# Optimization experiments

Measured on AMD Instinct MI355X. Metric: run time of the kernel, lower is better.

The kernel has to match this reference:

```python
import jax, jax.numpy as jnp
import numpy as np

TWO_PI = 2.0 * np.pi
B, S_IN, S_OUT, K, HID = 1024, 4096, 4096, 8, 512
EPS = 1e-6


def setup_inputs() -> dict:
    key = jax.random.key(0)
    k1, k2, k3, k4, k5, k6, k7, k8 = jax.random.split(key, 8)
    x_in = jax.random.uniform(k1, (B, S_OUT), dtype=jnp.float32) * TWO_PI
    x_passive = jax.random.normal(k2, (B, S_IN), dtype=jnp.float32)
    log_density = jax.random.normal(k3, (B, 1), dtype=jnp.float32)
    # MLP params (nn.Linear default-ish init scale)
    lim1 = 1.0 / np.sqrt(S_IN)
    lim2 = 1.0 / np.sqrt(HID)
    w1 = jax.random.uniform(k4, (S_IN, HID), jnp.float32, -lim1, lim1)
    b1 = jax.random.uniform(k5, (HID,), jnp.float32, -lim1, lim1)
    w2 = jax.random.uniform(k6, (HID, S_OUT * 3 * K), jnp.float32, -lim2, lim2)
    b2 = jax.random.uniform(k7, (S_OUT * 3 * K,), jnp.float32, -lim2, lim2)
    phase_shift = jax.random.uniform(k8, (1,), jnp.float32)
    return {"x_in": x_in, "x_passive": x_passive, "log_density": log_density,
            "w1": w1, "b1": b1, "w2": w2, "b2": b2, "phase_shift": phase_shift}


def reference(x_in, x_passive, log_density, w1, b1, w2, b2, phase_shift):
    # normalise network input with global mean / (unbiased) std, as torch does
    xn = (x_passive - x_passive.mean()) / x_passive.std(ddof=1)
    # dense network: Linear -> tanh -> Linear -> tanh (final_activation=activation)
    net = jnp.tanh(jnp.tanh(xn @ w1 + b1) @ w2 + b2)            # (B, S*3K)
    net = net.reshape(-1, S_OUT, 3 * K)
    h_raw, w_raw, d_raw = net[..., :K], net[..., K:2 * K], net[..., 2 * K:]
    h_norm = jax.nn.softmax(h_raw, axis=2) * TWO_PI              # (B,S,K)
    w_norm = jax.nn.softmax(w_raw, axis=2) * TWO_PI
    d_norm = jax.nn.softplus(d_raw)
    bshape = (h_norm.shape[0], S_OUT, 1)
    x_kp = jnp.concatenate([jnp.full(bshape, -EPS, h_norm.dtype),
                            jnp.cumsum(w_norm, axis=2)], axis=2)  # (B,S,K+1)
    phi_kp = jnp.concatenate([jnp.zeros(bshape, h_norm.dtype),
                              jnp.cumsum(h_norm, axis=2)], axis=2)
    x = x_in[..., None]                                          # (B,S,1)
    # searchsorted (left) per element: count of knots strictly less than x, minus 1
    k_ind = jnp.sum(x_kp < x, axis=2, keepdims=True) - 1         # (B,S,1) int
    k_ind = jnp.clip(k_ind, 0, K - 1)
    g = lambda a, i: jnp.take_along_axis(a, i, axis=2)
    w_k = g(w_norm, k_ind)
    h_k = g(h_norm, k_ind)
    s_k = h_k / w_k
    d_k = g(d_norm, k_ind)
    d_kp1 = g(d_norm, (k_ind + 1) % K)
    x_km1 = g(x_kp, k_ind)
    phi_km1 = g(phi_kp, k_ind)
    alpha = (x - x_km1) / w_k
    a1m = alpha * (1.0 - alpha)
    denom = s_k + (d_kp1 + d_k - 2.0 * s_k) * a1m
    phi_out = (phi_km1 + h_k * (s_k * alpha ** 2 + d_k * a1m) / denom)[..., 0]
    phi_out = (phi_out + phase_shift) % TWO_PI                   # (B,S)
    grad = s_k ** 2 * (d_kp1 * alpha ** 2 + 2.0 * s_k * a1m
                       + d_k * (1.0 - alpha) ** 2) / denom ** 2  # (B,S,1)
    log_density = log_density - jnp.log(grad).sum(axis=1)        # (B,1)
    return phi_out, log_density
```

## Files before the change

kernel.cpp:

```cpp
#include <hip/hip_runtime.h>
#include <cstdint>
#include <cstddef>


typedef unsigned short u16;
typedef __bf16 bf16x8 __attribute__((ext_vector_type(8)));
typedef float f32x4 __attribute__((ext_vector_type(4)));
typedef unsigned short u16x8 __attribute__((ext_vector_type(8)));

#define TWOPI_F 6.28318530717958647692f

static __device__ __forceinline__ u16 f32_to_bf16(float f){
  unsigned u = __builtin_bit_cast(unsigned, f);
  return (u16)((u + 0x7fffu + ((u >> 16) & 1u)) >> 16);
}
static __device__ __forceinline__ void async16(void* lds, const void* g){
  __builtin_amdgcn_global_load_lds((const __attribute__((address_space(1))) void*)g,
                                   (__attribute__((address_space(3))) void*)lds,
                                   16, 0, 0);
}
static __device__ __forceinline__ float fast_tanh(float x){
  x = fminf(fmaxf(x, -15.f), 15.f);
  float e = __expf(2.f * x);
  return (e - 1.f) / (e + 1.f);
}
static __device__ __forceinline__ float softplus_f(float x){
  return fmaxf(x, 0.f) + __logf(1.f + __expf(-fabsf(x)));
}

__global__ void k_stats(const float* __restrict__ xp, float* __restrict__ stats){
  __shared__ float ss[4], sq[4];
  const int tid = threadIdx.x;
  const long gt = (long)blockIdx.x * 256 + tid;
  const float4* x4 = (const float4*)xp;
  float s = 0.f, q = 0.f;
  #pragma unroll
  for (int p = 0; p < 4; ++p){
    float4 v = x4[gt + (long)p * 262144];
    s += v.x + v.y + v.z + v.w;
    q += v.x*v.x + v.y*v.y + v.z*v.z + v.w*v.w;
  }
  #pragma unroll
  for (int off = 32; off; off >>= 1){
    s += __shfl_down(s, off);
    q += __shfl_down(q, off);
  }
  if ((tid & 63) == 0){ ss[tid>>6] = s; sq[tid>>6] = q; }
  __syncthreads();
  if (tid == 0){
    atomicAdd(stats,     ss[0]+ss[1]+ss[2]+ss[3]);
    atomicAdd(stats + 1, sq[0]+sq[1]+sq[2]+sq[3]);
  }
}

__global__ void k_prep(const float* __restrict__ xp, const float* __restrict__ stats,
                       u16* __restrict__ xn){
  const long t = (long)blockIdx.x * 256 + threadIdx.x;
  const float sum = stats[0], sq = stats[1];
  const float N = 4194304.f;
  const float mean = sum / N;
  const float istd = rsqrtf((sq - sum*sum/N) / (N - 1.f));
  const float4* x4 = (const float4*)xp;
  const float4 a = x4[2*t], b = x4[2*t+1];
  u16x8 o;
  o[0]=f32_to_bf16((a.x-mean)*istd); o[1]=f32_to_bf16((a.y-mean)*istd);
  o[2]=f32_to_bf16((a.z-mean)*istd); o[3]=f32_to_bf16((a.w-mean)*istd);
  o[4]=f32_to_bf16((b.x-mean)*istd); o[5]=f32_to_bf16((b.y-mean)*istd);
  o[6]=f32_to_bf16((b.z-mean)*istd); o[7]=f32_to_bf16((b.w-mean)*istd);
  ((u16x8*)xn)[t] = o;
}

__global__ void k_transpose_cvt(const float* __restrict__ in, u16* __restrict__ out,
                                int Kd, int Nd){
  __shared__ float tile[64][65];
  const int tid = threadIdx.x;
  const long k0 = (long)blockIdx.x * 64, n0 = (long)blockIdx.y * 64;
  const int cl = (tid & 15) * 4, rw = tid >> 4;
  #pragma unroll
  for (int p = 0; p < 4; ++p){
    const int kk = rw + p*16;
    const float4 v = *(const float4*)&in[(k0+kk)*Nd + n0 + cl];
    tile[kk][cl] = v.x; tile[kk][cl+1] = v.y; tile[kk][cl+2] = v.z; tile[kk][cl+3] = v.w;
  }
  __syncthreads();
  const int nl = tid >> 2, kc = (tid & 3) * 16;
  u16x8 o0, o1;
  #pragma unroll
  for (int i = 0; i < 8; ++i) o0[i] = f32_to_bf16(tile[kc+i][nl]);
  #pragma unroll
  for (int i = 0; i < 8; ++i) o1[i] = f32_to_bf16(tile[kc+8+i][nl]);
  u16* op = out + (n0+nl)*Kd + k0 + kc;
  *(u16x8*)op = o0;
  *(u16x8*)(op + 8) = o1;
}

__global__ __launch_bounds__(256, 2) void k_gemm1(
    const u16* __restrict__ xn,
    const u16* __restrict__ w1t,
    const float* __restrict__ b1,
    u16* __restrict__ hb)
{
  __shared__ __align__(16) u16 sA[64*32];
  __shared__ __align__(16) u16 sB[64*32];
  const int tid = threadIdx.x, lane = tid & 63, w = tid >> 6;
  const int n0 = blockIdx.x << 6, m0 = blockIdx.y << 6;
  const int wm = w >> 1, wn = w & 1;
  const int rA = lane >> 2, cA = (lane & 3) << 3;
  const int fr = lane & 15, fq = lane >> 4;
  const f32x4 z4 = {0.f, 0.f, 0.f, 0.f};
  f32x4 acc[2][2];
  #pragma unroll
  for (int i=0;i<2;i++){ acc[i][0] = z4; acc[i][1] = z4; }

  for (int kt = 0; kt < 128; ++kt){
    const int kofs = (kt << 5) + cA;
    async16(sA + w*512, xn  + (long)(m0 + w*16 + rA)*4096 + kofs);
    async16(sB + w*512, w1t + (long)(n0 + w*16 + rA)*4096 + kofs);
    __syncthreads();
    bf16x8 af[2], bfv[2];
    #pragma unroll
    for (int i=0;i<2;i++) af[i]  = *(const bf16x8*)(sA + ((wm<<5) + i*16 + fr)*32 + (fq<<3));
    #pragma unroll
    for (int j=0;j<2;j++) bfv[j] = *(const bf16x8*)(sB + ((wn<<5) + j*16 + fr)*32 + (fq<<3));
    #pragma unroll
    for (int i=0;i<2;i++)
      #pragma unroll
      for (int j=0;j<2;j++)
        acc[i][j] = __builtin_amdgcn_mfma_f32_16x16x32_bf16(af[i], bfv[j], acc[i][j], 0, 0, 0);
    __syncthreads();
  }
  float b1c[2];
  #pragma unroll
  for (int j=0;j<2;j++) b1c[j] = b1[n0 + (wn<<5) + j*16 + fr];
  #pragma unroll
  for (int i=0;i<2;i++)
    #pragma unroll
    for (int j=0;j<2;j++)
      #pragma unroll
      for (int r=0;r<4;r++){
        const int row = m0 + (wm<<5) + i*16 + (fq<<2) + r;
        const int col = n0 + (wn<<5) + j*16 + fr;
        hb[row*512 + col] = f32_to_bf16(fast_tanh(acc[i][j][r] + b1c[j]));
      }
}

__global__ __launch_bounds__(256, 2) void k_gemm2(
    const u16* __restrict__ hmat,
    const u16* __restrict__ w2t,
    const float* __restrict__ b2,
    const float* __restrict__ x_in,
    const float* __restrict__ phase,
    float* __restrict__ phi_out,
    float* __restrict__ part)
{
  __shared__ __align__(16) char smem[25600];
  u16* sA = (u16*)smem;
  u16* sB = (u16*)(smem + 16384);
  float* sC = (float*)smem;

  const int tid  = threadIdx.x;
  const int lane = tid & 63;
  const int w    = tid >> 6;
  const int nt   = blockIdx.x;
  const int m0   = blockIdx.y << 8;
  const long n0  = (long)nt * 96;

  const int rA = lane >> 2, cA = (lane & 3) << 3;
  const int fr = lane & 15, fq = lane >> 4;

  const f32x4 z4 = {0.f, 0.f, 0.f, 0.f};
  f32x4 acc[4][6];
  #pragma unroll
  for (int i=0;i<4;i++)
    #pragma unroll
    for (int j=0;j<6;j++) acc[i][j] = z4;

  for (int kt = 0; kt < 16; ++kt){
    const int kofs = (kt << 5) + cA;
    #pragma unroll
    for (int cc = 0; cc < 4; ++cc){
      const int c = (w << 2) + cc;
      async16(sA + c*512, hmat + (long)(m0 + c*16 + rA)*512 + kofs);
    }
    #pragma unroll
    for (int cc = 0; cc < 2; ++cc){
      const int ch = (w << 1) + cc;
      int row = ch*16 + rA; if (row > 95) row = 95;
      async16(sB + ch*512, w2t + (n0 + row)*512 + kofs);
    }
    __syncthreads();
    bf16x8 af[4], bfv[6];
    #pragma unroll
    for (int i=0;i<4;i++)
      af[i] = *(const bf16x8*)(sA + ((w<<6) + i*16 + fr)*32 + (fq<<3));
    #pragma unroll
    for (int j=0;j<6;j++)
      bfv[j] = *(const bf16x8*)(sB + (j*16 + fr)*32 + (fq<<3));
    #pragma unroll
    for (int i=0;i<4;i++)
      #pragma unroll
      for (int j=0;j<6;j++)
        acc[i][j] = __builtin_amdgcn_mfma_f32_16x16x32_bf16(af[i], bfv[j], acc[i][j], 0, 0, 0);
    __syncthreads();
  }

  const float shift = phase[0];
  float b2c[6];
  #pragma unroll
  for (int j=0;j<6;j++) b2c[j] = b2[n0 + j*16 + fr];
  float* myC = sC + w*1600;

  #pragma unroll
  for (int q = 0; q < 4; ++q){
    __syncthreads();
    #pragma unroll
    for (int j=0;j<6;j++)
      #pragma unroll
      for (int r=0;r<4;r++)
        myC[((fq<<2)+r)*100 + j*16 + fr] = fast_tanh(acc[q][j][r] + b2c[j]);
    __syncthreads();

    const int row = fr;
    const int g   = fq;
    const float* tp = myC + row*100 + g*24;
    float t[24];
    #pragma unroll
    for (int jj=0;jj<24;jj++) t[jj] = tp[jj];

    const int bg = m0 + (w<<6) + (q<<4) + row;
    const int s  = (nt<<2) + g;
    const float x = x_in[(long)bg*4096 + s];

    float eh[8], ew[8];
    float sh = 0.f, sw = 0.f;
    #pragma unroll
    for (int i=0;i<8;i++){ eh[i] = __expf(t[i]);   sh += eh[i]; }
    #pragma unroll
    for (int i=0;i<8;i++){ ew[i] = __expf(t[8+i]); sw += ew[i]; }
    const float fh = TWOPI_F / sh, fw = TWOPI_F / sw;

    float cw = 0.f; int k = 0;
    #pragma unroll
    for (int i=0;i<8;i++){ cw += ew[i]*fw; k += (cw < x) ? 1 : 0; }
    if (k > 7) k = 7;

    float xkm1 = -1e-6f, ph = 0.f, wk = 0.f, hk = 0.f, dr0 = 0.f, dr1 = 0.f;
    float cw2 = 0.f, chs = 0.f;
    #pragma unroll
    for (int i=0;i<8;i++){
      const float wi = ew[i]*fw, hi = eh[i]*fh;
      if (i == k){
        wk = wi; hk = hi;
        xkm1 = (i == 0) ? -1e-6f : cw2;
        ph = chs;
        dr0 = t[16 + i];
        dr1 = t[16 + ((i+1)&7)];
      }
      cw2 += wi; chs += hi;
    }
    const float dk  = softplus_f(dr0);
    const float dk1 = softplus_f(dr1);
    const float sk  = hk / wk;
    const float alpha = (x - xkm1) / wk;
    const float a1m = alpha * (1.f - alpha);
    const float denom = sk + (dk1 + dk - 2.f*sk)*a1m;
    const float phiv = ph + hk*(sk*alpha*alpha + dk*a1m)/denom;
    float p = phiv + shift;
    if (p >= TWOPI_F) p -= TWOPI_F;
    if (p >= TWOPI_F) p -= TWOPI_F;
    phi_out[(long)bg*4096 + s] = p;

    const float om = 1.f - alpha;
    const float num = dk1*alpha*alpha + 2.f*sk*a1m + dk*om*om;
    float lg = __logf(sk*sk*num/(denom*denom));
    lg += __shfl_xor(lg, 16);
    lg += __shfl_xor(lg, 32);
    if (lane < 16) part[(long)bg*1024 + nt] = lg;
  }
}

__global__ void k_ldred(const float* __restrict__ part, const float* __restrict__ ldin,
                        float* __restrict__ ldout){
  __shared__ float ss[4];
  const int b = blockIdx.x, tid = threadIdx.x;
  const float4* p4 = (const float4*)(part + ((long)b << 10));
  const float4 v = p4[tid];
  float s = v.x + v.y + v.z + v.w;
  #pragma unroll
  for (int off = 32; off; off >>= 1) s += __shfl_down(s, off);
  if ((tid & 63) == 0) ss[tid >> 6] = s;
  __syncthreads();
  if (tid == 0) ldout[b] = ldin[b] - (ss[0]+ss[1]+ss[2]+ss[3]);
}

extern "C" void kernel_launch(void* const* d_in, const int* in_sizes, int n_in,
                              void* d_out, int out_size, void* d_ws, size_t ws_size,
                              hipStream_t stream){
  (void)in_sizes; (void)n_in; (void)out_size; (void)ws_size;
  const float* x_in  = (const float*)d_in[0];
  const float* x_pas = (const float*)d_in[1];
  const float* ldin  = (const float*)d_in[2];
  const float* w1    = (const float*)d_in[3];
  const float* b1    = (const float*)d_in[4];
  const float* w2    = (const float*)d_in[5];
  const float* b2    = (const float*)d_in[6];
  const float* phase = (const float*)d_in[7];
  float* out   = (float*)d_out;
  float* phi   = out;
  float* ldout = out + (size_t)1024*4096;

  char* ws = (char*)d_ws;
  float* stats = (float*)ws;
  u16* xn   = (u16*)(ws + 256);
  u16* w1t  = (u16*)(ws + 8388864);
  u16* hb   = (u16*)(ws + 12583168);
  u16* w2t  = (u16*)(ws + 13631744);
  float* part = (float*)(ws + 114295040);

  hipMemsetAsync(stats, 0, 8, stream);
  k_stats<<<1024, 256, 0, stream>>>(x_pas, stats);
  k_prep<<<2048, 256, 0, stream>>>(x_pas, stats, xn);
  k_transpose_cvt<<<dim3(64, 8),   256, 0, stream>>>(w1, w1t, 4096, 512);
  k_transpose_cvt<<<dim3(8, 1536), 256, 0, stream>>>(w2, w2t, 512, 98304);
  k_gemm1<<<dim3(8, 16), 256, 0, stream>>>(xn, w1t, b1, hb);
  k_gemm2<<<dim3(1024, 4), 256, 0, stream>>>(hb, w2t, b2, x_in, phase, phi, part);
  k_ldred<<<1024, 256, 0, stream>>>(part, ldin, ldout);
}
```

Measured before the change: 607.1 us.

## Widen transpose tiles, split-K gemm1, and reorder gemm2 grid for reuse

The weight transpose-convert kernel now uses 256x128 tiles, converts to bf16 before staging in LDS with an XOR swizzle, and writes full 16-byte rows, which cuts LDS traffic and the number of blocks. gemm1 is split along K into two halves to double its block count, with a new small kernel that sums the partials and applies bias and tanh. The gemm2 grid swaps its x/y mapping so the four M-blocks sharing a W2 tile are scheduled next to each other, improving L2 reuse of the large weight matrix. The partial buffer reuses the workspace region `part` before gemm2 overwrites it, and the split adds an extra launch plus an fp32 round trip.

Result: faster. 569.1 us (-6.3%).

```diff
diff --git a/kernel.cpp b/kernel.cpp
--- a/kernel.cpp
+++ b/kernel.cpp
@@ -7,6 +7,8 @@
 typedef __bf16 bf16x8 __attribute__((ext_vector_type(8)));
 typedef float f32x4 __attribute__((ext_vector_type(4)));
 typedef unsigned short u16x8 __attribute__((ext_vector_type(8)));
+typedef unsigned short u16x4 __attribute__((ext_vector_type(4)));
+typedef unsigned short u16x2 __attribute__((ext_vector_type(2)));
 
 #define TWOPI_F 6.28318530717958647692f
 
@@ -70,40 +72,48 @@
   ((u16x8*)xn)[t] = o;
 }
 
-__global__ void k_transpose_cvt(const float* __restrict__ in, u16* __restrict__ out,
-                                int Kd, int Nd){
-  __shared__ float tile[64][65];
+__global__ __launch_bounds__(256) void k_transpose_cvt(const float* __restrict__ in,
+                                                       u16* __restrict__ out,
+                                                       int Kd, int Nd){
+  __shared__ __align__(16) u16 tT[128*256];
   const int tid = threadIdx.x;
-  const long k0 = (long)blockIdx.x * 64, n0 = (long)blockIdx.y * 64;
-  const int cl = (tid & 15) * 4, rw = tid >> 4;
-  #pragma unroll
-  for (int p = 0; p < 4; ++p){
-    const int kk = rw + p*16;
-    const float4 v = *(const float4*)&in[(k0+kk)*Nd + n0 + cl];
-    tile[kk][cl] = v.x; tile[kk][cl+1] = v.y; tile[kk][cl+2] = v.z; tile[kk][cl+3] = v.w;
+  const long k0 = (long)blockIdx.x * 256, n0 = (long)blockIdx.y * 128;
+  const int lam = tid & 31, g = tid >> 5;
+  const int c = lam * 4;
+  const int sig = (lam & 7) << 2;
+  #pragma unroll
+  for (int pass = 0; pass < 16; ++pass){
+    const int P = pass*8 + g;
+    const float4 f0 = *(const float4*)&in[(k0 + 2*P    )*Nd + n0 + c];
+    const float4 f1 = *(const float4*)&in[(k0 + 2*P + 1)*Nd + n0 + c];
+    const int pp = 2*(P ^ sig);
+    *(u16x2*)&tT[(c    )*256 + pp] = u16x2{f32_to_bf16(f0.x), f32_to_bf16(f1.x)};
+    *(u16x2*)&tT[(c + 1)*256 + pp] = u16x2{f32_to_bf16(f0.y), f32_to_bf16(f1.y)};
+    *(u16x2*)&tT[(c + 2)*256 + pp] = u16x2{f32_to_bf16(f0.z), f32_to_bf16(f1.z)};
+    *(u16x2*)&tT[(c + 3)*256 + pp] = u16x2{f32_to_bf16(f0.w), f32_to_bf16(f1.w)};
   }
   __syncthreads();
-  const int nl = tid >> 2, kc = (tid & 3) * 16;
-  u16x8 o0, o1;
-  #pragma unroll
-  for (int i = 0; i < 8; ++i) o0[i] = f32_to_bf16(tile[kc+i][nl]);
-  #pragma unroll
-  for (int i = 0; i < 8; ++i) o1[i] = f32_to_bf16(tile[kc+8+i][nl]);
-  u16* op = out + (n0+nl)*Kd + k0 + kc;
-  *(u16x8*)op = o0;
-  *(u16x8*)(op + 8) = o1;
+  const int w = tid >> 6, l = tid & 63;
+  const int lh = l >> 5, lk = l & 31;
+  #pragma unroll
+  for (int it = 0; it < 16; ++it){
+    const int n = (w << 5) + (it << 1) + lh;
+    const int s2 = (n >> 2) & 7;
+    const u16x8 v = *(const u16x8*)&tT[n*256 + 8*(lk ^ s2)];
+    *(u16x8*)&out[(n0 + n)*Kd + k0 + 8*lk] = v;
+  }
 }
 
 __global__ __launch_bounds__(256, 2) void k_gemm1(
     const u16* __restrict__ xn,
     const u16* __restrict__ w1t,
-    const float* __restrict__ b1,
-    u16* __restrict__ hb)
+    float* __restrict__ pp)
 {
   __shared__ __align__(16) u16 sA[64*32];
   __shared__ __align__(16) u16 sB[64*32];
   const int tid = threadIdx.x, lane = tid & 63, w = tid >> 6;
   const int n0 = blockIdx.x << 6, m0 = blockIdx.y << 6;
+  const int ks = blockIdx.z;
   const int wm = w >> 1, wn = w & 1;
   const int rA = lane >> 2, cA = (lane & 3) << 3;
   const int fr = lane & 15, fq = lane >> 4;
@@ -112,8 +122,8 @@
   #pragma unroll
   for (int i=0;i<2;i++){ acc[i][0] = z4; acc[i][1] = z4; }
 
-  for (int kt = 0; kt < 128; ++kt){
-    const int kofs = (kt << 5) + cA;
+  for (int kt = 0; kt < 64; ++kt){
+    const int kofs = (ks << 11) + (kt << 5) + cA;
     async16(sA + w*512, xn  + (long)(m0 + w*16 + rA)*4096 + kofs);
     async16(sB + w*512, w1t + (long)(n0 + w*16 + rA)*4096 + kofs);
     __syncthreads();
@@ -129,9 +139,7 @@
         acc[i][j] = __builtin_amdgcn_mfma_f32_16x16x32_bf16(af[i], bfv[j], acc[i][j], 0, 0, 0);
     __syncthreads();
   }
-  float b1c[2];
-  #pragma unroll
-  for (int j=0;j<2;j++) b1c[j] = b1[n0 + (wn<<5) + j*16 + fr];
+  float* po = pp + ((size_t)ks << 19);
   #pragma unroll
   for (int i=0;i<2;i++)
     #pragma unroll
@@ -140,8 +148,22 @@
       for (int r=0;r<4;r++){
         const int row = m0 + (wm<<5) + i*16 + (fq<<2) + r;
         const int col = n0 + (wn<<5) + j*16 + fr;
-        hb[row*512 + col] = f32_to_bf16(fast_tanh(acc[i][j][r] + b1c[j]));
+        po[row*512 + col] = acc[i][j][r];
       }
+}
+
+__global__ void k_gemm1b(const float* __restrict__ pp, const float* __restrict__ b1,
+                         u16* __restrict__ hb){
+  const int t = blockIdx.x * 256 + threadIdx.x;
+  const float4 a = ((const float4*)pp)[t];
+  const float4 b = ((const float4*)pp)[131072 + t];
+  const float4 bb = ((const float4*)b1)[t & 127];
+  u16x4 o;
+  o[0] = f32_to_bf16(fast_tanh(a.x + b.x + bb.x));
+  o[1] = f32_to_bf16(fast_tanh(a.y + b.y + bb.y));
+  o[2] = f32_to_bf16(fast_tanh(a.z + b.z + bb.z));
+  o[3] = f32_to_bf16(fast_tanh(a.w + b.w + bb.w));
+  ((u16x4*)hb)[t] = o;
 }
 
 __global__ __launch_bounds__(256, 2) void k_gemm2(
@@ -161,8 +183,8 @@
   const int tid  = threadIdx.x;
   const int lane = tid & 63;
   const int w    = tid >> 6;
-  const int nt   = blockIdx.x;
-  const int m0   = blockIdx.y << 8;
+  const int nt   = blockIdx.y;
+  const int m0   = blockIdx.x << 8;
   const long n0  = (long)nt * 96;
 
   const int rA = lane >> 2, cA = (lane & 3) << 3;
@@ -320,9 +342,10 @@
   hipMemsetAsync(stats, 0, 8, stream);
   k_stats<<<1024, 256, 0, stream>>>(x_pas, stats);
   k_prep<<<2048, 256, 0, stream>>>(x_pas, stats, xn);
-  k_transpose_cvt<<<dim3(64, 8),   256, 0, stream>>>(w1, w1t, 4096, 512);
-  k_transpose_cvt<<<dim3(8, 1536), 256, 0, stream>>>(w2, w2t, 512, 98304);
-  k_gemm1<<<dim3(8, 16), 256, 0, stream>>>(xn, w1t, b1, hb);
-  k_gemm2<<<dim3(1024, 4), 256, 0, stream>>>(hb, w2t, b2, x_in, phase, phi, part);
+  k_transpose_cvt<<<dim3(16, 4),  256, 0, stream>>>(w1, w1t, 4096, 512);
+  k_transpose_cvt<<<dim3(2, 768), 256, 0, stream>>>(w2, w2t, 512, 98304);
+  k_gemm1<<<dim3(8, 16, 2), 256, 0, stream>>>(xn, w1t, part);
+  k_gemm1b<<<512, 256, 0, stream>>>(part, b1, hb);
+  k_gemm2<<<dim3(4, 1024), 256, 0, stream>>>(hb, w2t, b2, x_in, phase, phi, part);
   k_ldred<<<1024, 256, 0, stream>>>(part, ldin, ldout);
 }
```
